# Optimization experiments

Hardware: AMD Instinct MI355X
Metric: run time of the kernel (lower is better)

The kernel has to match this reference:

```python
import jax, jax.numpy as jnp
import numpy as np

N = 50000          # nodes
E = 1000000        # edges (avg degree 20)
F_IN = 16          # fluidFeatures
LAYERS = [64, 64, 64, 2]
TERMS = 4          # basisTerms
DIM = 2            # spatial dim
EDGE_DIM = TERMS * DIM  # mode='cat' -> terms * dim = 8
OUT_SCALE = 1.0 / 128.0  # outputScaling


def fourier_basis(n_terms, x):
    """Fourier basis ('ffourier'): k=0 -> 1, odd k -> sin(pi*ceil(k/2)*x), even k -> cos(pi*(k/2)*x). x: [E] -> [E, n_terms]."""
    cols = []
    for k in range(n_terms):
        if k == 0:
            cols.append(jnp.ones_like(x))
        elif k % 2 == 1:
            cols.append(jnp.sin(jnp.pi * ((k + 1) // 2) * x))
        else:
            cols.append(jnp.cos(jnp.pi * (k // 2) * x))
    return jnp.stack(cols, axis=-1)


def edge_basis(edge_lengths):
    # basisEncoderLayer with mode='cat': per-component basis, concatenated -> [E, TERMS*DIM]
    return jnp.concatenate([fourier_basis(TERMS, edge_lengths[:, d]) for d in range(DIM)], axis=1)


def setup_inputs() -> dict:
    key = jax.random.key(0)
    k_x, k_ei, k_el, k_w = jax.random.split(key, 4)
    x = jax.random.normal(k_x, (N, F_IN), dtype=jnp.float32)
    edge_index = jax.random.randint(k_ei, (2, E), 0, N)
    edge_lengths = jax.random.uniform(k_el, (E, DIM), dtype=jnp.float32, minval=-1.0, maxval=1.0)
    # continuous-conv weights: [EDGE_DIM, in_feat, out_feat] per layer (uniform-style init)
    weights = {}
    in_f = F_IN
    wkeys = jax.random.split(k_w, len(LAYERS))
    for i, out_f in enumerate(LAYERS):
        scale = 1.0 / np.sqrt(EDGE_DIM * in_f)
        weights[f"W{i}"] = scale * jax.random.normal(wkeys[i], (EDGE_DIM, in_f, out_f), dtype=jnp.float32)
        in_f = out_f
    return dict(x=x, edge_index=edge_index, edge_lengths=edge_lengths, **weights)


def reference(x, edge_index, edge_lengths, W0, W1, W2, W3):
    src = edge_index[0]
    dst = edge_index[1]
    basis = edge_basis(edge_lengths)            # [E, EDGE_DIM]
    Ws = [W0, W1, W2, W3]
    h = x
    for i, W in enumerate(Ws):
        # gather sender features, contract with per-edge basis and conv weight, scatter-sum to receivers
        msg = jnp.einsum('eb,ef,bfo->eo', basis, h[src], W)   # [E, out]
        agg = jax.ops.segment_sum(msg, dst, num_segments=N)   # [N, out]
        h = jax.nn.relu(agg) if i < len(Ws) - 1 else agg
    return h * OUT_SCALE
```

## Files before the change

### kernel.cpp

```cpp
#include <hip/hip_runtime.h>
#include <hip/hip_bf16.h>
#include <math.h>

#define PI_F 3.14159265358979323846f

typedef __attribute__((ext_vector_type(8))) short bf16x8;
typedef __attribute__((ext_vector_type(4))) float f32x4;
typedef __attribute__((ext_vector_type(4))) unsigned short u16x4;
typedef __attribute__((ext_vector_type(8))) unsigned short u16x8;

__device__ __forceinline__ float bf2f(unsigned short u) {
    union { unsigned int i; float f; } v;
    v.i = ((unsigned int)u) << 16;
    return v.f;
}

__device__ __forceinline__ unsigned short f2bf_bits(float f) {
    __hip_bfloat16 b = __float2bfloat16(f);
    unsigned short u;
    __builtin_memcpy(&u, &b, 2);
    return u;
}


__global__ void count_kernel(const int* __restrict__ dst, int* __restrict__ cnt, int E) {
    int e = blockIdx.x * 256 + threadIdx.x;
    if (e < E) atomicAdd(&cnt[dst[e]], 1);
}

__global__ __launch_bounds__(256) void scan_reduce_kernel(const int* __restrict__ cnt,
                                                          int* __restrict__ bsum, int n) {
    __shared__ int sd[4];
    int idx = blockIdx.x * 256 + threadIdx.x;
    int v = (idx < n) ? cnt[idx] : 0;
    int s = v;
#pragma unroll
    for (int m = 1; m < 64; m <<= 1) s += __shfl_xor(s, m, 64);
    int wave = threadIdx.x >> 6;
    if ((threadIdx.x & 63) == 0) sd[wave] = s;
    __syncthreads();
    if (threadIdx.x == 0) bsum[blockIdx.x] = sd[0] + sd[1] + sd[2] + sd[3];
}

__global__ __launch_bounds__(256) void scan_top_kernel(const int* __restrict__ bsum,
                                                       int* __restrict__ boffs, int nb) {
    __shared__ int sd[256];
    int tid = threadIdx.x;
    int v = (tid < nb) ? bsum[tid] : 0;
    sd[tid] = v;
    __syncthreads();
#pragma unroll
    for (int off = 1; off < 256; off <<= 1) {
        int t = (tid >= off) ? sd[tid - off] : 0;
        __syncthreads();
        sd[tid] += t;
        __syncthreads();
    }
    if (tid < nb) boffs[tid] = sd[tid] - v;
}

__global__ __launch_bounds__(256) void scan_apply_kernel(int* __restrict__ cntcur,
                                                         int* __restrict__ offs,
                                                         const int* __restrict__ boffs,
                                                         int n, int total) {
    __shared__ int sd[256];
    int tid = threadIdx.x;
    int idx = blockIdx.x * 256 + tid;
    int v = (idx < n) ? cntcur[idx] : 0;
    sd[tid] = v;
    __syncthreads();
#pragma unroll
    for (int off = 1; off < 256; off <<= 1) {
        int t = (tid >= off) ? sd[tid - off] : 0;
        __syncthreads();
        sd[tid] += t;
        __syncthreads();
    }
    if (idx < n) {
        int ex = boffs[blockIdx.x] + sd[tid] - v;
        offs[idx] = ex;
        cntcur[idx] = ex;
    }
    if (idx == 0) offs[n] = total;
}

__global__ void fill_kernel(const int* __restrict__ src, const int* __restrict__ dst,
                            const float* __restrict__ el, int* __restrict__ cursor,
                            int* __restrict__ srcS, unsigned short* __restrict__ basisB, int E) {
    int e = blockIdx.x * 256 + threadIdx.x;
    if (e >= E) return;
    int d = dst[e];
    int pos = atomicAdd(&cursor[d], 1);
    srcS[pos] = src[e];
    float2 xy = *(const float2*)(el + 2 * (size_t)e);
    u16x8 p;
    p[0] = f2bf_bits(1.0f);
    p[1] = f2bf_bits(__sinf(PI_F * xy.x));
    p[2] = f2bf_bits(__cosf(PI_F * xy.x));
    p[3] = f2bf_bits(__sinf(2.0f * PI_F * xy.x));
    p[4] = f2bf_bits(1.0f);
    p[5] = f2bf_bits(__sinf(PI_F * xy.y));
    p[6] = f2bf_bits(__cosf(PI_F * xy.y));
    p[7] = f2bf_bits(__sinf(2.0f * PI_F * xy.y));
    *(u16x8*)(basisB + (size_t)pos * 8) = p;
}


__global__ void prep_w_kernel(const float* __restrict__ W, __hip_bfloat16* __restrict__ Wt, int K) {
    int i = blockIdx.x * 256 + threadIdx.x;
    if (i >= K * 64) return;
    int k = i >> 6, o = i & 63;
    Wt[(size_t)o * K + k] = __float2bfloat16(W[i]);
}

__global__ void prep_f2b_kernel(const float* __restrict__ in, __hip_bfloat16* __restrict__ out, int n) {
    int i = blockIdx.x * 256 + threadIdx.x;
    if (i < n) out[i] = __float2bfloat16(in[i]);
}


__device__ __forceinline__ void agg64_core(const unsigned short* __restrict__ hp,
                                           const int* __restrict__ srcS,
                                           const unsigned short* __restrict__ basisB,
                                           int start, int end, int eg, int fb,
                                           float acc[8][4]) {
    const int last = end - 1;
    int j = start;
    int qa = min(j + eg, last), qb = min(j + 4 + eg, last);
    int sa = srcS[qa], sb = srcS[qb];
    u16x4 ga = *(const u16x4*)(hp + (size_t)sa * 64 + fb);
    u16x4 gb = *(const u16x4*)(hp + (size_t)sb * 64 + fb);
    u16x8 ca = *(const u16x8*)(basisB + (size_t)qa * 8);
    u16x8 cb = *(const u16x8*)(basisB + (size_t)qb * 8);
    int qna = min(j + 8 + eg, last), qnb = min(j + 12 + eg, last);
    int sna = srcS[qna], snb = srcS[qnb];
    while (true) {
        int jn = j + 8;
        int q2a = min(jn + 8 + eg, last), q2b = min(jn + 12 + eg, last);
        int s2a = srcS[q2a], s2b = srcS[q2b];
        u16x4 gna = *(const u16x4*)(hp + (size_t)sna * 64 + fb);
        u16x4 gnb = *(const u16x4*)(hp + (size_t)snb * 64 + fb);
        u16x8 cna = *(const u16x8*)(basisB + (size_t)qna * 8);
        u16x8 cnb = *(const u16x8*)(basisB + (size_t)qnb * 8);
        float ha[4], hb[4];
        ha[0] = bf2f(ga[0]); ha[1] = bf2f(ga[1]); ha[2] = bf2f(ga[2]); ha[3] = bf2f(ga[3]);
        hb[0] = bf2f(gb[0]); hb[1] = bf2f(gb[1]); hb[2] = bf2f(gb[2]); hb[3] = bf2f(gb[3]);
        if (j + eg >= end)     { ha[0] = 0.f; ha[1] = 0.f; ha[2] = 0.f; ha[3] = 0.f; }
        if (j + 4 + eg >= end) { hb[0] = 0.f; hb[1] = 0.f; hb[2] = 0.f; hb[3] = 0.f; }
#pragma unroll
        for (int b = 0; b < 8; b++) {
            float w = bf2f(ca[b]);
#pragma unroll
            for (int c = 0; c < 4; c++) acc[b][c] += w * ha[c];
        }
#pragma unroll
        for (int b = 0; b < 8; b++) {
            float w = bf2f(cb[b]);
#pragma unroll
            for (int c = 0; c < 4; c++) acc[b][c] += w * hb[c];
        }
        if (jn >= end) break;
        j = jn;
        ga = gna; gb = gnb; ca = cna; cb = cnb;
        qna = q2a; qnb = q2b; sna = s2a; snb = s2b;
    }
}

__global__ __launch_bounds__(256) void agg64_kernel(const __hip_bfloat16* __restrict__ h,
                                                    const int* __restrict__ srcS,
                                                    const unsigned short* __restrict__ basisB,
                                                    const int* __restrict__ offs,
                                                    __hip_bfloat16* __restrict__ A, int nN) {
    int wid = (blockIdx.x * 256 + threadIdx.x) >> 6;
    int lane = threadIdx.x & 63;
    if (wid >= nN) return;
    int eg = lane >> 4, fg = lane & 15;
    int start = offs[wid], end = offs[wid + 1];
    float acc[8][4] = {};
    if (start < end)
        agg64_core((const unsigned short*)h, srcS, basisB, start, end, eg, fg * 4, acc);
#pragma unroll
    for (int b = 0; b < 8; b++) {
#pragma unroll
        for (int c = 0; c < 4; c++) {
            float v = acc[b][c];
            v += __shfl_xor(v, 16, 64);
            v += __shfl_xor(v, 32, 64);
            acc[b][c] = v;
        }
    }
    if (eg == 0) {
        unsigned short* Ar = (unsigned short*)A + (size_t)wid * 512;
#pragma unroll
        for (int b = 0; b < 8; b++) {
            u16x4 p;
            p[0] = f2bf_bits(acc[b][0]); p[1] = f2bf_bits(acc[b][1]);
            p[2] = f2bf_bits(acc[b][2]); p[3] = f2bf_bits(acc[b][3]);
            *(u16x4*)(Ar + b * 64 + fg * 4) = p;
        }
    }
}

__global__ __launch_bounds__(256) void agg_out_kernel(const __hip_bfloat16* __restrict__ h,
                                                      const int* __restrict__ srcS,
                                                      const unsigned short* __restrict__ basisB,
                                                      const int* __restrict__ offs,
                                                      const float* __restrict__ W3,
                                                      float* __restrict__ out, int nN) {
    int wid = (blockIdx.x * 256 + threadIdx.x) >> 6;
    int lane = threadIdx.x & 63;
    if (wid >= nN) return;
    int eg = lane >> 4, fg = lane & 15;
    int start = offs[wid], end = offs[wid + 1];
    float acc[8][4] = {};
    if (start < end)
        agg64_core((const unsigned short*)h, srcS, basisB, start, end, eg, fg * 4, acc);
#pragma unroll
    for (int b = 0; b < 8; b++) {
#pragma unroll
        for (int c = 0; c < 4; c++) {
            float v = acc[b][c];
            v += __shfl_xor(v, 16, 64);
            v += __shfl_xor(v, 32, 64);
            acc[b][c] = v;
        }
    }
    float o0 = 0.f, o1 = 0.f;
#pragma unroll
    for (int b = 0; b < 8; b++) {
        const float* w = W3 + (size_t)(b * 64 + fg * 4) * 2;
        float4 wa = *(const float4*)w;
        float4 wb = *(const float4*)(w + 4);
        o0 += acc[b][0] * wa.x + acc[b][1] * wa.z + acc[b][2] * wb.x + acc[b][3] * wb.z;
        o1 += acc[b][0] * wa.y + acc[b][1] * wa.w + acc[b][2] * wb.y + acc[b][3] * wb.w;
    }
#pragma unroll
    for (int m = 1; m < 16; m <<= 1) {
        o0 += __shfl_xor(o0, m, 64);
        o1 += __shfl_xor(o1, m, 64);
    }
    if (lane == 0) {
        out[(size_t)wid * 2 + 0] = o0 * (1.0f / 128.0f);
        out[(size_t)wid * 2 + 1] = o1 * (1.0f / 128.0f);
    }
}


__global__ __launch_bounds__(256) void agg16_kernel(const __hip_bfloat16* __restrict__ h,
                                                    const int* __restrict__ srcS,
                                                    const unsigned short* __restrict__ basisB,
                                                    const int* __restrict__ offs,
                                                    __hip_bfloat16* __restrict__ A, int nN) {
    int wid = (blockIdx.x * 256 + threadIdx.x) >> 6;
    int lane = threadIdx.x & 63;
    if (wid >= nN) return;
    int eg = lane >> 2, fg = lane & 3;
    int start = offs[wid], end = offs[wid + 1];
    float acc[8][4] = {};
    if (start < end) {
        const unsigned short* hp = (const unsigned short*)h;
        const int last = end - 1;
        const int fb = fg * 4;
        int j = start;
        int q = min(j + eg, last);
        int s = srcS[q];
        u16x4 g = *(const u16x4*)(hp + (size_t)s * 16 + fb);
        u16x8 cbv = *(const u16x8*)(basisB + (size_t)q * 8);
        int qn = min(j + 16 + eg, last);
        int sn = srcS[qn];
        while (true) {
            int jn = j + 16;
            int q2 = min(jn + 16 + eg, last);
            int s2 = srcS[q2];
            u16x4 gn = *(const u16x4*)(hp + (size_t)sn * 16 + fb);
            u16x8 cn = *(const u16x8*)(basisB + (size_t)qn * 8);
            float hv[4];
            hv[0] = bf2f(g[0]); hv[1] = bf2f(g[1]); hv[2] = bf2f(g[2]); hv[3] = bf2f(g[3]);
            if (j + eg >= end) { hv[0] = 0.f; hv[1] = 0.f; hv[2] = 0.f; hv[3] = 0.f; }
#pragma unroll
            for (int b = 0; b < 8; b++) {
                float w = bf2f(cbv[b]);
#pragma unroll
                for (int c = 0; c < 4; c++) acc[b][c] += w * hv[c];
            }
            if (jn >= end) break;
            j = jn;
            g = gn; cbv = cn; qn = q2; sn = s2;
        }
    }
#pragma unroll
    for (int b = 0; b < 8; b++) {
#pragma unroll
        for (int c = 0; c < 4; c++) {
            float v = acc[b][c];
            v += __shfl_xor(v, 4, 64);
            v += __shfl_xor(v, 8, 64);
            v += __shfl_xor(v, 16, 64);
            v += __shfl_xor(v, 32, 64);
            acc[b][c] = v;
        }
    }
    if (eg == 0) {
        unsigned short* Ar = (unsigned short*)A + (size_t)wid * 128;
#pragma unroll
        for (int b = 0; b < 8; b++) {
            u16x4 p;
            p[0] = f2bf_bits(acc[b][0]); p[1] = f2bf_bits(acc[b][1]);
            p[2] = f2bf_bits(acc[b][2]); p[3] = f2bf_bits(acc[b][3]);
            *(u16x4*)(Ar + b * 16 + fg * 4) = p;
        }
    }
}


template <int K, bool RELU>
__global__ __launch_bounds__(256) void gemm_mfma_kernel(const __hip_bfloat16* __restrict__ A,
                                                        const __hip_bfloat16* __restrict__ Wt,
                                                        __hip_bfloat16* __restrict__ Hout, int nN) {
    int wave = threadIdx.x >> 6;
    int lane = threadIdx.x & 63;
    int m16 = lane & 15;
    int kg = lane >> 4;
    int arow = blockIdx.x * 64 + wave * 16 + m16;
    bool rowok = arow < nN;
    const short* Ap = (const short*)A;
    const short* Wp = (const short*)Wt;
    size_t abase = (size_t)arow * K + kg * 8;
    size_t wb0 = (size_t)(0 * 16 + m16) * K + kg * 8;
    size_t wb1 = (size_t)(1 * 16 + m16) * K + kg * 8;
    size_t wb2 = (size_t)(2 * 16 + m16) * K + kg * 8;
    size_t wb3 = (size_t)(3 * 16 + m16) * K + kg * 8;
    f32x4 acc0 = {0.f, 0.f, 0.f, 0.f};
    f32x4 acc1 = {0.f, 0.f, 0.f, 0.f};
    f32x4 acc2 = {0.f, 0.f, 0.f, 0.f};
    f32x4 acc3 = {0.f, 0.f, 0.f, 0.f};
#pragma unroll 4
    for (int kc = 0; kc < K; kc += 32) {
        bf16x8 af = {};
        if (rowok) af = *(const bf16x8*)(Ap + abase + kc);
        bf16x8 b0 = *(const bf16x8*)(Wp + wb0 + kc);
        bf16x8 b1 = *(const bf16x8*)(Wp + wb1 + kc);
        bf16x8 b2 = *(const bf16x8*)(Wp + wb2 + kc);
        bf16x8 b3 = *(const bf16x8*)(Wp + wb3 + kc);
        acc0 = __builtin_amdgcn_mfma_f32_16x16x32_bf16(af, b0, acc0, 0, 0, 0);
        acc1 = __builtin_amdgcn_mfma_f32_16x16x32_bf16(af, b1, acc1, 0, 0, 0);
        acc2 = __builtin_amdgcn_mfma_f32_16x16x32_bf16(af, b2, acc2, 0, 0, 0);
        acc3 = __builtin_amdgcn_mfma_f32_16x16x32_bf16(af, b3, acc3, 0, 0, 0);
    }
    int orow0 = blockIdx.x * 64 + wave * 16 + kg * 4;
#pragma unroll
    for (int r = 0; r < 4; r++) {
        int row = orow0 + r;
        if (row < nN) {
            float v0 = acc0[r], v1 = acc1[r], v2 = acc2[r], v3 = acc3[r];
            if (RELU) {
                v0 = fmaxf(v0, 0.0f); v1 = fmaxf(v1, 0.0f);
                v2 = fmaxf(v2, 0.0f); v3 = fmaxf(v3, 0.0f);
            }
            __hip_bfloat16* Hr = Hout + (size_t)row * 64;
            Hr[0 * 16 + m16] = __float2bfloat16(v0);
            Hr[1 * 16 + m16] = __float2bfloat16(v1);
            Hr[2 * 16 + m16] = __float2bfloat16(v2);
            Hr[3 * 16 + m16] = __float2bfloat16(v3);
        }
    }
}


extern "C" void kernel_launch(void* const* d_in, const int* in_sizes, int n_in,
                              void* d_out, int out_size, void* d_ws, size_t ws_size,
                              hipStream_t stream) {
    const float* x  = (const float*)d_in[0];
    const int*   ei = (const int*)d_in[1];
    const float* el = (const float*)d_in[2];
    const float* W0 = (const float*)d_in[3];
    const float* W1 = (const float*)d_in[4];
    const float* W2 = (const float*)d_in[5];
    const float* W3 = (const float*)d_in[6];
    int nN = in_sizes[0] / 16;
    int E  = in_sizes[1] / 2;
    const int* src = ei;
    const int* dst = ei + E;

    char* ws = (char*)d_ws;
    size_t off = 0;
    auto alloc = [&](size_t bytes) -> void* {
        void* p = ws + off;
        off = (off + bytes + 255) & ~(size_t)255;
        return p;
    };
    int nsb = (nN + 255) / 256;
    int*   cntcur = (int*)alloc((size_t)(nN + 1) * 4);
    int*   offs   = (int*)alloc((size_t)(nN + 1) * 4);
    int*   bsum   = (int*)alloc((size_t)nsb * 4);
    int*   boffs  = (int*)alloc((size_t)nsb * 4);
    int*   srcS   = (int*)alloc((size_t)E * 4);
    unsigned short* basisB = (unsigned short*)alloc((size_t)E * 8 * 2);
    __hip_bfloat16* Ab  = (__hip_bfloat16*)alloc((size_t)nN * 512 * 2);
    __hip_bfloat16* Wt0 = (__hip_bfloat16*)alloc((size_t)64 * 128 * 2);
    __hip_bfloat16* Wt1 = (__hip_bfloat16*)alloc((size_t)64 * 512 * 2);
    __hip_bfloat16* Wt2 = (__hip_bfloat16*)alloc((size_t)64 * 512 * 2);
    __hip_bfloat16* xb  = (__hip_bfloat16*)alloc((size_t)nN * 16 * 2);
    __hip_bfloat16* hA  = (__hip_bfloat16*)alloc((size_t)nN * 64 * 2);
    __hip_bfloat16* hB  = (__hip_bfloat16*)alloc((size_t)nN * 64 * 2);
    (void)ws_size;

    hipMemsetAsync(cntcur, 0, (size_t)nN * 4, stream);
    int eb = (E + 255) / 256;
    count_kernel<<<eb, 256, 0, stream>>>(dst, cntcur, E);
    scan_reduce_kernel<<<nsb, 256, 0, stream>>>(cntcur, bsum, nN);
    scan_top_kernel<<<1, 256, 0, stream>>>(bsum, boffs, nsb);
    scan_apply_kernel<<<nsb, 256, 0, stream>>>(cntcur, offs, boffs, nN, E);
    fill_kernel<<<eb, 256, 0, stream>>>(src, dst, el, cntcur, srcS, basisB, E);

    prep_w_kernel<<<(128 * 64 + 255) / 256, 256, 0, stream>>>(W0, Wt0, 128);
    prep_w_kernel<<<(512 * 64 + 255) / 256, 256, 0, stream>>>(W1, Wt1, 512);
    prep_w_kernel<<<(512 * 64 + 255) / 256, 256, 0, stream>>>(W2, Wt2, 512);
    prep_f2b_kernel<<<(nN * 16 + 255) / 256, 256, 0, stream>>>(x, xb, nN * 16);

    int nb = (nN + 3) / 4;
    int gb = (nN + 63) / 64;

    agg16_kernel<<<nb, 256, 0, stream>>>(xb, srcS, basisB, offs, Ab, nN);
    gemm_mfma_kernel<128, true><<<gb, 256, 0, stream>>>(Ab, Wt0, hA, nN);
    agg64_kernel<<<nb, 256, 0, stream>>>(hA, srcS, basisB, offs, Ab, nN);
    gemm_mfma_kernel<512, true><<<gb, 256, 0, stream>>>(Ab, Wt1, hB, nN);
    agg64_kernel<<<nb, 256, 0, stream>>>(hB, srcS, basisB, offs, Ab, nN);
    gemm_mfma_kernel<512, true><<<gb, 256, 0, stream>>>(Ab, Wt2, hA, nN);
    agg_out_kernel<<<nb, 256, 0, stream>>>(hA, srcS, basisB, offs, W3, (float*)d_out, nN);
}
```

Baseline: 432.6 us.

## Replace global-atomic CSR fill with two-pass bucketed counting sort

```diff
diff --git a/kernel.cpp b/kernel.cpp
--- a/kernel.cpp
+++ b/kernel.cpp
@@ -3,6 +3,9 @@
 #include <math.h>
 
 #define PI_F 3.14159265358979323846f
+#define BK_SHIFT 8
+#define P2_CHUNK 4096
+#define P2_PER_THREAD 16
 
 typedef __attribute__((ext_vector_type(8))) short bf16x8;
 typedef __attribute__((ext_vector_type(4))) float f32x4;
@@ -76,33 +79,106 @@
         sd[tid] += t;
         __syncthreads();
     }
-    if (idx < n) {
-        int ex = boffs[blockIdx.x] + sd[tid] - v;
-        offs[idx] = ex;
-        cntcur[idx] = ex;
-    }
+    if (idx < n) offs[idx] = boffs[blockIdx.x] + sd[tid] - v;
     if (idx == 0) offs[n] = total;
 }
 
-__global__ void fill_kernel(const int* __restrict__ src, const int* __restrict__ dst,
-                            const float* __restrict__ el, int* __restrict__ cursor,
-                            int* __restrict__ srcS, unsigned short* __restrict__ basisB, int E) {
-    int e = blockIdx.x * 256 + threadIdx.x;
-    if (e >= E) return;
-    int d = dst[e];
-    int pos = atomicAdd(&cursor[d], 1);
-    srcS[pos] = src[e];
-    float2 xy = *(const float2*)(el + 2 * (size_t)e);
-    u16x8 p;
-    p[0] = f2bf_bits(1.0f);
-    p[1] = f2bf_bits(__sinf(PI_F * xy.x));
-    p[2] = f2bf_bits(__cosf(PI_F * xy.x));
-    p[3] = f2bf_bits(__sinf(2.0f * PI_F * xy.x));
-    p[4] = f2bf_bits(1.0f);
-    p[5] = f2bf_bits(__sinf(PI_F * xy.y));
-    p[6] = f2bf_bits(__cosf(PI_F * xy.y));
-    p[7] = f2bf_bits(__sinf(2.0f * PI_F * xy.y));
-    *(u16x8*)(basisB + (size_t)pos * 8) = p;
+__global__ void bucket_init_kernel(const int* __restrict__ offs, int* __restrict__ bucketCursor,
+                                   int nbuk, int nN) {
+    int b = blockIdx.x * 256 + threadIdx.x;
+    if (b < nbuk) bucketCursor[b] = offs[min(b << BK_SHIFT, nN)];
+}
+
+__global__ __launch_bounds__(256) void bucket_scatter_kernel(const int* __restrict__ dst,
+                                                             int* __restrict__ bucketCursor,
+                                                             int* __restrict__ inter,
+                                                             int E, int nbuk) {
+    __shared__ int lcnt[256];
+    __shared__ int lbase[256];
+    __shared__ int lgpos[256];
+    __shared__ int lsort[P2_CHUNK];
+    __shared__ unsigned char lbuk[P2_CHUNK];
+    int tid = threadIdx.x;
+    int base = blockIdx.x * P2_CHUNK;
+    lcnt[tid] = 0;
+    __syncthreads();
+    int myb[P2_PER_THREAD], myr[P2_PER_THREAD];
+#pragma unroll
+    for (int i = 0; i < P2_PER_THREAD; i++) {
+        int idx = base + i * 256 + tid;
+        int b = -1, r = 0;
+        if (idx < E) {
+            b = dst[idx] >> BK_SHIFT;
+            r = atomicAdd(&lcnt[b], 1);
+        }
+        myb[i] = b;
+        myr[i] = r;
+    }
+    __syncthreads();
+    int v = lcnt[tid];
+    lbase[tid] = v;
+    __syncthreads();
+    for (int off = 1; off < 256; off <<= 1) {
+        int t = (tid >= off) ? lbase[tid - off] : 0;
+        __syncthreads();
+        lbase[tid] += t;
+        __syncthreads();
+    }
+    int excl = lbase[tid] - v;
+    if (tid < nbuk && v > 0) lgpos[tid] = atomicAdd(&bucketCursor[tid], v);
+    __syncthreads();
+    lbase[tid] = excl;
+    __syncthreads();
+#pragma unroll
+    for (int i = 0; i < P2_PER_THREAD; i++) {
+        if (myb[i] >= 0) {
+            int p = lbase[myb[i]] + myr[i];
+            lsort[p] = base + i * 256 + tid;
+            lbuk[p] = (unsigned char)myb[i];
+        }
+    }
+    __syncthreads();
+    int total = (base + P2_CHUNK <= E) ? P2_CHUNK : (E > base ? E - base : 0);
+    for (int idx = tid; idx < total; idx += 256) {
+        int b = lbuk[idx];
+        inter[lgpos[b] + (idx - lbase[b])] = lsort[idx];
+    }
+}
+
+__global__ __launch_bounds__(256) void bucket_sort_fill_kernel(const int* __restrict__ inter,
+                                                               const int* __restrict__ dst,
+                                                               const int* __restrict__ src,
+                                                               const float* __restrict__ el,
+                                                               const int* __restrict__ offs,
+                                                               int* __restrict__ srcS,
+                                                               unsigned short* __restrict__ basisB,
+                                                               int nN) {
+    __shared__ int cursor[256];
+    int b = blockIdx.x;
+    int n0 = b << BK_SHIFT;
+    int n1 = min(n0 + 256, nN);
+    int tid = threadIdx.x;
+    int p0 = offs[n0];
+    int p1 = offs[n1];
+    if (tid < n1 - n0) cursor[tid] = offs[n0 + tid];
+    __syncthreads();
+    for (int q = p0 + tid; q < p1; q += 256) {
+        int e = inter[q];
+        int d = dst[e];
+        int pos = atomicAdd(&cursor[d - n0], 1);
+        srcS[pos] = src[e];
+        float2 xy = *(const float2*)(el + 2 * (size_t)e);
+        u16x8 p;
+        p[0] = f2bf_bits(1.0f);
+        p[1] = f2bf_bits(__sinf(PI_F * xy.x));
+        p[2] = f2bf_bits(__cosf(PI_F * xy.x));
+        p[3] = f2bf_bits(__sinf(2.0f * PI_F * xy.x));
+        p[4] = f2bf_bits(1.0f);
+        p[5] = f2bf_bits(__sinf(PI_F * xy.y));
+        p[6] = f2bf_bits(__cosf(PI_F * xy.y));
+        p[7] = f2bf_bits(__sinf(2.0f * PI_F * xy.y));
+        *(u16x8*)(basisB + (size_t)pos * 8) = p;
+    }
 }
 
 
@@ -389,11 +465,14 @@
         off = (off + bytes + 255) & ~(size_t)255;
         return p;
     };
-    int nsb = (nN + 255) / 256;
+    int nsb  = (nN + 255) / 256;
+    int nbuk = (nN + 255) >> BK_SHIFT;
     int*   cntcur = (int*)alloc((size_t)(nN + 1) * 4);
     int*   offs   = (int*)alloc((size_t)(nN + 1) * 4);
     int*   bsum   = (int*)alloc((size_t)nsb * 4);
     int*   boffs  = (int*)alloc((size_t)nsb * 4);
+    int*   bukcur = (int*)alloc((size_t)nbuk * 4);
+    int*   inter  = (int*)alloc((size_t)E * 4);
     int*   srcS   = (int*)alloc((size_t)E * 4);
     unsigned short* basisB = (unsigned short*)alloc((size_t)E * 8 * 2);
     __hip_bfloat16* Ab  = (__hip_bfloat16*)alloc((size_t)nN * 512 * 2);
@@ -411,7 +490,10 @@
     scan_reduce_kernel<<<nsb, 256, 0, stream>>>(cntcur, bsum, nN);
     scan_top_kernel<<<1, 256, 0, stream>>>(bsum, boffs, nsb);
     scan_apply_kernel<<<nsb, 256, 0, stream>>>(cntcur, offs, boffs, nN, E);
-    fill_kernel<<<eb, 256, 0, stream>>>(src, dst, el, cntcur, srcS, basisB, E);
+    bucket_init_kernel<<<(nbuk + 255) / 256, 256, 0, stream>>>(offs, bukcur, nbuk, nN);
+    int p2b = (E + P2_CHUNK - 1) / P2_CHUNK;
+    bucket_scatter_kernel<<<p2b, 256, 0, stream>>>(dst, bukcur, inter, E, nbuk);
+    bucket_sort_fill_kernel<<<nbuk, 256, 0, stream>>>(inter, dst, src, el, offs, srcS, basisB, nN);
 
     prep_w_kernel<<<(128 * 64 + 255) / 256, 256, 0, stream>>>(W0, Wt0, 128);
     prep_w_kernel<<<(512 * 64 + 255) / 256, 256, 0, stream>>>(W1, Wt1, 512);
```

Measured after the change: 418.7 us. 1.03x faster.
